# Performance work log

Hardware: AMD Instinct MI355X
Metric: run time of the kernel (lower is better)

The kernel has to match this reference:

```python
import jax, jax.numpy as jnp
import numpy as np

B, D, O = 16384, 1024, 2048
MU, LAM = 0.9, 0.1


def setup_inputs() -> dict:
    key = jax.random.key(0)
    ks = jax.random.split(key, 16)
    stdv = float(1.0 / np.sqrt(D))
    u = lambda k, shape, s: jax.random.uniform(k, shape, jnp.float32, -s, s)
    return {
        "x": jax.random.normal(ks[0], (B, D), jnp.float32),
        "x_ctx": jax.random.normal(ks[1], (B, D), jnp.float32),
        "classifier": u(ks[2], (O, D), stdv),
        "none_tensor": u(ks[3], (1, D), stdv),
        "ctx_q_w": u(ks[4], (O, D), stdv),
        "ctx_q_b": u(ks[5], (O,), stdv),
        "word_g_w": u(ks[6], (1, D), stdv),
        "word_g_b": u(ks[7], (1,), stdv),
        "tcq_w1": u(ks[8], (D, D), stdv),
        "tcq_b1": u(ks[9], (D,), stdv),
        "tcq_w2": u(ks[10], (O, D), stdv),
        "tcq_b2": u(ks[11], (O,), stdv),
        "history_input": 0.1 * jax.random.normal(ks[12], (O - 1, D), jnp.float32),
        "history_count": jax.random.randint(ks[13], (O - 1,), 0, 10),
        "labels": jax.random.randint(ks[14], (B,), 0, O),
    }


def reference(x, x_ctx, classifier, none_tensor, ctx_q_w, ctx_q_b,
              word_g_w, word_g_b, tcq_w1, tcq_b1, tcq_w2, tcq_b2,
              history_input, history_count, labels):
    mu, lam = MU, LAM
    # ---- update_history (torch.no_grad), vectorized over classes via segment_sum ----
    xs = jax.lax.stop_gradient(x)
    sums = jax.ops.segment_sum(xs, labels, num_segments=O)               # [O, D]
    counts = jax.ops.segment_sum(jnp.ones((B,), jnp.float32), labels, num_segments=O)  # [O]
    has = counts[1:] > 0                                                  # classes 1..O-1
    cls_mean = sums[1:] / jnp.maximum(counts[1:], 1.0)[:, None]
    hist = jnp.where(has[:, None], mu * history_input + cls_mean, history_input)
    cnt = history_count + has.astype(history_count.dtype)
    # ---- generate_substitute (mu < 1 branch) ----
    denom = 1.0 - jnp.power(mu, jnp.maximum(cnt, 1).astype(jnp.float32))[:, None]
    v = hist * (1.0 - mu) / denom                                        # [O-1, D]
    r_sub = jnp.concatenate([none_tensor, v], axis=0)                    # [O, D]
    ctx_logits = x_ctx @ ctx_q_w.T + ctx_q_b                              # [B, O]
    att_logits = jax.nn.gelu(x @ tcq_w1.T + tcq_b1, approximate=False) @ tcq_w2.T + tcq_b2  # [B, O]
    # ---- gated combine + bilinear classifier (training=True path: w uses ctx_logits) ----
    g_word = jax.nn.sigmoid(x @ word_g_w.T + word_g_b)                    # [B, 1]
    w = g_word * jax.nn.sigmoid(ctx_logits)                               # [B, O]
    # logits = sum(((1-w)*x[:,None,:] + w*r_sub) * classifier, -1), collapsed algebraically
    logits = (1.0 - w) * (x @ classifier.T) + w * jnp.einsum('od,od->o', r_sub, classifier)[None, :]
    # ---- losses on labels >= 0 (mask-weighted means, jit-safe) ----
    mask = (labels >= 0).astype(jnp.float32)
    n = jnp.maximum(mask.sum(), 1.0)
    lsm = jax.nn.log_softmax(logits, axis=-1)
    nll = -jnp.take_along_axis(lsm, jnp.maximum(labels, 0)[:, None], axis=1)[:, 0]
    ce = (mask * nll).sum() / n
    mse_row = jnp.mean((ctx_logits - att_logits) ** 2, axis=-1)
    mse = (mask * mse_row).sum() / n
    return (ce + lam * mse, logits)
```

## Files before the change

kernel.cpp:

```cpp
#include <hip/hip_runtime.h>
#include <cstdint>
#include <cstddef>

#define DEV __device__ __forceinline__

typedef __attribute__((ext_vector_type(4))) float f32x4;
typedef __attribute__((ext_vector_type(8))) short bf16x8;
typedef unsigned short ushort_t;
typedef __attribute__((ext_vector_type(8))) unsigned short ushort8;

static constexpr int B_ = 16384, D_ = 1024, O_ = 2048;
static constexpr float LAM_ = 0.1f;

static constexpr size_t WS_XBF   = 0;
static constexpr size_t WS_XCBF  = WS_XBF   + (size_t)B_ * D_ * 2;
static constexpr size_t WS_HBF   = WS_XCBF  + (size_t)B_ * D_ * 2;
static constexpr size_t WS_CLSBF = WS_HBF   + (size_t)B_ * D_ * 2;
static constexpr size_t WS_CTWBF = WS_CLSBF + (size_t)O_ * D_ * 2;
static constexpr size_t WS_W2BF  = WS_CTWBF + (size_t)O_ * D_ * 2;
static constexpr size_t WS_W1BF  = WS_W2BF  + (size_t)O_ * D_ * 2;
static constexpr size_t WS_SMALL = WS_W1BF  + (size_t)D_ * D_ * 2;
static constexpr size_t SM_COUNTS = 0;
static constexpr size_t SM_TSUM   = 8192;
static constexpr size_t SM_MSE    = 16384;
static constexpr size_t SM_ACCS   = 81920;
static constexpr size_t SM_ZERO_BYTES = 82176;
static constexpr size_t SM_S      = 82176;
static constexpr size_t SM_GWORD  = 90368;
static constexpr size_t SM_CEROW  = 155904;

DEV float wave_sum(float v) {
  #pragma unroll
  for (int o = 32; o; o >>= 1) v += __shfl_xor(v, o, 64);
  return v;
}

DEV ushort_t f2bf1(float f) {
  union { float f; unsigned u; } c{f};
  unsigned r = c.u + 0x7fffu + ((c.u >> 16) & 1u);
  return (ushort_t)(r >> 16);
}

DEV float sigmoidf(float z) { return 1.0f / (1.0f + expf(-z)); }

DEV void gload_lds16(const ushort_t* g, ushort_t* l) {
  __builtin_amdgcn_global_load_lds((const __attribute__((address_space(1))) void*)g,
                                   (__attribute__((address_space(3))) void*)l, 16, 0, 0);
}

DEV void stage_tile(const ushort_t* __restrict__ src, size_t ldk, ushort_t* lds, int tid) {
  int c0 = tid, c1 = tid + 256;
  gload_lds16(src + (size_t)(c0 >> 2) * ldk + (size_t)((c0 & 3) * 8), lds + c0 * 8);
  gload_lds16(src + (size_t)(c1 >> 2) * ldk + (size_t)((c1 & 3) * 8), lds + c1 * 8);
}

__global__ __launch_bounds__(256) void f2bf_kernel(const float* __restrict__ in,
                                                   ushort_t* __restrict__ out, int n8) {
  int i = blockIdx.x * 256 + threadIdx.x;
  if (i >= n8) return;
  const float4* p = (const float4*)(in + (size_t)i * 8);
  float4 a = p[0], b = p[1];
  ushort8 o;
  o[0] = f2bf1(a.x); o[1] = f2bf1(a.y); o[2] = f2bf1(a.z); o[3] = f2bf1(a.w);
  o[4] = f2bf1(b.x); o[5] = f2bf1(b.y); o[6] = f2bf1(b.z); o[7] = f2bf1(b.w);
  *(ushort8*)(out + (size_t)i * 8) = o;
}

__global__ __launch_bounds__(256) void rowdot_kernel(const float* __restrict__ x,
    const float* __restrict__ cls, const float* __restrict__ wg,
    const float* __restrict__ wgb, const int* __restrict__ labels,
    float* __restrict__ tsum, float* __restrict__ counts, float* __restrict__ g_word) {
  int wave = threadIdx.x >> 6, lane = threadIdx.x & 63;
  int row = blockIdx.x * 4 + wave;
  const float* xr = x + (size_t)row * D_;
  int lab = labels[row];
  const float* cr = cls + (size_t)max(lab, 0) * D_;
  float t = 0.f, g = 0.f;
  #pragma unroll
  for (int j = 0; j < 4; ++j) {
    int d = j * 256 + lane * 4;
    float4 xv = *(const float4*)(xr + d);
    float4 cv = *(const float4*)(cr + d);
    float4 wv = *(const float4*)(wg + d);
    t += xv.x * cv.x + xv.y * cv.y + xv.z * cv.z + xv.w * cv.w;
    g += xv.x * wv.x + xv.y * wv.y + xv.z * wv.z + xv.w * wv.w;
  }
  t = wave_sum(t); g = wave_sum(g);
  if (lane == 0) {
    if (lab >= 0) {
      atomicAdd(&tsum[lab], t);
      atomicAdd(&counts[lab], 1.0f);
    }
    g_word[row] = sigmoidf(g + wgb[0]);
  }
}

__global__ __launch_bounds__(256) void scls_kernel(const float* __restrict__ cls,
    const float* __restrict__ none_t, const float* __restrict__ hist,
    const int* __restrict__ hcnt, const float* __restrict__ counts,
    const float* __restrict__ tsum, float* __restrict__ s) {
  int wave = threadIdx.x >> 6, lane = threadIdx.x & 63;
  int o = blockIdx.x * 4 + wave;
  if (o >= O_) return;
  const float* cr = cls + (size_t)o * D_;
  const float* src = (o == 0) ? none_t : hist + (size_t)(o - 1) * D_;
  float dv = 0.f;
  #pragma unroll
  for (int j = 0; j < 4; ++j) {
    int d = j * 256 + lane * 4;
    float4 a = *(const float4*)(src + d);
    float4 c = *(const float4*)(cr + d);
    dv += a.x * c.x + a.y * c.y + a.z * c.z + a.w * c.w;
  }
  dv = wave_sum(dv);
  if (lane == 0) {
    if (o == 0) { s[0] = dv; }
    else {
      float co = counts[o];
      bool has = co > 0.f;
      int cnt = hcnt[o - 1] + (has ? 1 : 0);
      float denom = 1.f - powf(0.9f, (float)max(cnt, 1));
      float val = has ? (0.9f * dv + tsum[o] / fmaxf(co, 1.f)) : dv;
      s[o] = (0.1f / denom) * val;
    }
  }
}

__global__ __launch_bounds__(256, 3) void gemm_h_kernel(const ushort_t* __restrict__ A,
    const ushort_t* __restrict__ Bw, const float* __restrict__ bias,
    ushort_t* __restrict__ Hout) {
  __shared__ ushort_t As[128 * 32], Bs[128 * 32];
  const int tid = threadIdx.x, lane = tid & 63, wave = tid >> 6;
  const int wr = wave >> 1, wc = wave & 1;
  int bid = blockIdx.x;
  int group = bid / 64, within = bid % 64;
  int bm = group * 8 + (within % 8);
  int bn = within / 8;
  f32x4 acc[4][4] = {};
  const ushort_t* Ap = A + (size_t)bm * 128 * D_;
  const ushort_t* Bp = Bw + (size_t)bn * 128 * D_;
  for (int k0 = 0; k0 < D_; k0 += 32) {
    stage_tile(Ap + k0, D_, As, tid);
    stage_tile(Bp + k0, D_, Bs, tid);
    __syncthreads();
    bf16x8 af[4], bfr[4];
    int r = lane & 15, kq = (lane >> 4) * 8;
    #pragma unroll
    for (int m = 0; m < 4; m++) af[m] = *(const bf16x8*)&As[(wr * 64 + m * 16 + r) * 32 + kq];
    #pragma unroll
    for (int n = 0; n < 4; n++) bfr[n] = *(const bf16x8*)&Bs[(wc * 64 + n * 16 + r) * 32 + kq];
    #pragma unroll
    for (int m = 0; m < 4; m++)
      #pragma unroll
      for (int n = 0; n < 4; n++)
        acc[m][n] = __builtin_amdgcn_mfma_f32_16x16x32_bf16(af[m], bfr[n], acc[m][n], 0, 0, 0);
    __syncthreads();
  }
  #pragma unroll
  for (int m = 0; m < 4; m++)
    #pragma unroll
    for (int n = 0; n < 4; n++) {
      int col = bn * 128 + wc * 64 + n * 16 + (lane & 15);
      float bcol = bias[col];
      #pragma unroll
      for (int i = 0; i < 4; i++) {
        int row = bm * 128 + wr * 64 + m * 16 + (lane >> 4) * 4 + i;
        float v = acc[m][n][i] + bcol;
        float gl = 0.5f * v * (1.f + erff(v * 0.70710678118f));
        Hout[(size_t)row * D_ + col] = f2bf1(gl);
      }
    }
}

__global__ __launch_bounds__(256, 3) void gemm_xc_kernel(const ushort_t* __restrict__ A,
    const ushort_t* __restrict__ Bw, float* __restrict__ out1) {
  __shared__ ushort_t As[128 * 32], Bs[128 * 32];
  const int tid = threadIdx.x, lane = tid & 63, wave = tid >> 6;
  const int wr = wave >> 1, wc = wave & 1;
  int bid = blockIdx.x;
  int group = bid / 128, within = bid % 128;
  int bm = group * 8 + (within % 8);
  int bn = within / 8;
  f32x4 acc[4][4] = {};
  const ushort_t* Ap = A + (size_t)bm * 128 * D_;
  const ushort_t* Bp = Bw + (size_t)bn * 128 * D_;
  for (int k0 = 0; k0 < D_; k0 += 32) {
    stage_tile(Ap + k0, D_, As, tid);
    stage_tile(Bp + k0, D_, Bs, tid);
    __syncthreads();
    bf16x8 af[4], bfr[4];
    int r = lane & 15, kq = (lane >> 4) * 8;
    #pragma unroll
    for (int m = 0; m < 4; m++) af[m] = *(const bf16x8*)&As[(wr * 64 + m * 16 + r) * 32 + kq];
    #pragma unroll
    for (int n = 0; n < 4; n++) bfr[n] = *(const bf16x8*)&Bs[(wc * 64 + n * 16 + r) * 32 + kq];
    #pragma unroll
    for (int m = 0; m < 4; m++)
      #pragma unroll
      for (int n = 0; n < 4; n++)
        acc[m][n] = __builtin_amdgcn_mfma_f32_16x16x32_bf16(af[m], bfr[n], acc[m][n], 0, 0, 0);
    __syncthreads();
  }
  #pragma unroll
  for (int m = 0; m < 4; m++)
    #pragma unroll
    for (int n = 0; n < 4; n++) {
      int col = bn * 128 + wc * 64 + n * 16 + (lane & 15);
      #pragma unroll
      for (int i = 0; i < 4; i++) {
        int row = bm * 128 + wr * 64 + m * 16 + (lane >> 4) * 4 + i;
        out1[(size_t)row * O_ + col] = acc[m][n][i];
      }
    }
}

__global__ __launch_bounds__(256, 2) void gemm_fused_kernel(
    const ushort_t* __restrict__ Axc,
    const ushort_t* __restrict__ Bctx,
    const ushort_t* __restrict__ Ah,
    const ushort_t* __restrict__ Batt,
    const float* __restrict__ ctx_b, const float* __restrict__ b2,
    const float* __restrict__ g_word, const float* __restrict__ s,
    float* __restrict__ mse_row, float* __restrict__ out1) {
  __shared__ ushort_t As1[128 * 32], Bs1[128 * 32], As2[128 * 32], Bs2[128 * 32];
  const int tid = threadIdx.x, lane = tid & 63, wave = tid >> 6;
  const int wr = wave >> 1, wc = wave & 1;
  int bid = blockIdx.x;
  int group = bid / 128, within = bid % 128;
  int bm = group * 8 + (within % 8);
  int bn = within / 8;
  f32x4 acc1[4][4] = {}, acc2[4][4] = {};
  const ushort_t* Ap1 = Axc + (size_t)bm * 128 * D_;
  const ushort_t* Bp1 = Bctx + (size_t)bn * 128 * D_;
  const ushort_t* Ap2 = Ah + (size_t)bm * 128 * D_;
  const ushort_t* Bp2 = Batt + (size_t)bn * 128 * D_;
  for (int k0 = 0; k0 < D_; k0 += 32) {
    stage_tile(Ap1 + k0, D_, As1, tid);
    stage_tile(Bp1 + k0, D_, Bs1, tid);
    stage_tile(Ap2 + k0, D_, As2, tid);
    stage_tile(Bp2 + k0, D_, Bs2, tid);
    __syncthreads();
    int r = lane & 15, kq = (lane >> 4) * 8;
    bf16x8 a1[4], b1v[4], a2[4], b2v[4];
    #pragma unroll
    for (int m = 0; m < 4; m++) {
      a1[m] = *(const bf16x8*)&As1[(wr * 64 + m * 16 + r) * 32 + kq];
      a2[m] = *(const bf16x8*)&As2[(wr * 64 + m * 16 + r) * 32 + kq];
    }
    #pragma unroll
    for (int n = 0; n < 4; n++) {
      b1v[n] = *(const bf16x8*)&Bs1[(wc * 64 + n * 16 + r) * 32 + kq];
      b2v[n] = *(const bf16x8*)&Bs2[(wc * 64 + n * 16 + r) * 32 + kq];
    }
    #pragma unroll
    for (int m = 0; m < 4; m++)
      #pragma unroll
      for (int n = 0; n < 4; n++) {
        acc1[m][n] = __builtin_amdgcn_mfma_f32_16x16x32_bf16(a1[m], b1v[n], acc1[m][n], 0, 0, 0);
        acc2[m][n] = __builtin_amdgcn_mfma_f32_16x16x32_bf16(a2[m], b2v[n], acc2[m][n], 0, 0, 0);
      }
    __syncthreads();
  }
  #pragma unroll
  for (int m = 0; m < 4; m++) {
    #pragma unroll
    for (int i = 0; i < 4; i++) {
      int row = bm * 128 + wr * 64 + m * 16 + (lane >> 4) * 4 + i;
      float gw = g_word[row];
      float msum = 0.f;
      #pragma unroll
      for (int n = 0; n < 4; n++) {
        int col = bn * 128 + wc * 64 + n * 16 + (lane & 15);
        float ctx = acc1[m][n][i] + ctx_b[col];
        float att = acc2[m][n][i] + b2[col];
        float w = gw * sigmoidf(ctx);
        size_t off = (size_t)row * O_ + col;
        float xc = out1[off];
        out1[off] = (1.f - w) * xc + w * s[col];
        float d = ctx - att;
        msum += d * d;
      }
      #pragma unroll
      for (int o = 1; o < 16; o <<= 1) msum += __shfl_xor(msum, o, 64);
      if ((lane & 15) == 0) atomicAdd(&mse_row[row], msum);
    }
  }
}

__global__ __launch_bounds__(256) void ce_kernel(const float* __restrict__ logits,
    const int* __restrict__ labels, float* __restrict__ ce_row) {
  int row = blockIdx.x, t = threadIdx.x, lane = t & 63, wave = t >> 6;
  const float* lr = logits + (size_t)row * O_;
  float v[8];
  float m = -INFINITY;
  #pragma unroll
  for (int j = 0; j < 8; j++) { v[j] = lr[t + j * 256]; m = fmaxf(m, v[j]); }
  #pragma unroll
  for (int o = 32; o; o >>= 1) m = fmaxf(m, __shfl_xor(m, o, 64));
  __shared__ float red[8];
  if (lane == 0) red[wave] = m;
  __syncthreads();
  m = fmaxf(fmaxf(red[0], red[1]), fmaxf(red[2], red[3]));
  float se = 0.f;
  #pragma unroll
  for (int j = 0; j < 8; j++) se += expf(v[j] - m);
  se = wave_sum(se);
  if (lane == 0) red[4 + wave] = se;
  __syncthreads();
  if (t == 0) {
    float bs = red[4] + red[5] + red[6] + red[7];
    int lab = labels[row];
    float nll = 0.f;
    if (lab >= 0) nll = -(lr[lab] - m - logf(bs));
    ce_row[row] = nll;
  }
}

__global__ __launch_bounds__(256) void finalize_kernel(const float* __restrict__ ce_row,
    const float* __restrict__ mse_row, const int* __restrict__ labels,
    float* __restrict__ out0) {
  int t = threadIdx.x, lane = t & 63, wave = t >> 6;
  float sn = 0.f, sm = 0.f, sc = 0.f;
  for (int i = t; i < B_; i += 256) {
    if (labels[i] >= 0) { sn += ce_row[i]; sm += mse_row[i]; sc += 1.f; }
  }
  sn = wave_sum(sn); sm = wave_sum(sm); sc = wave_sum(sc);
  __shared__ float r0[4], r1[4], r2[4];
  if (lane == 0) { r0[wave] = sn; r1[wave] = sm; r2[wave] = sc; }
  __syncthreads();
  if (t == 0) {
    float a = r0[0] + r0[1] + r0[2] + r0[3];
    float b = r1[0] + r1[1] + r1[2] + r1[3];
    float c = r2[0] + r2[1] + r2[2] + r2[3];
    out0[0] = (a + LAM_ * (b / (float)O_)) / fmaxf(c, 1.f);
  }
}

extern "C" void kernel_launch(void* const* d_in, const int* in_sizes, int n_in,
                              void* d_out, int out_size, void* d_ws, size_t ws_size,
                              hipStream_t stream) {
  const float* x        = (const float*)d_in[0];
  const float* x_ctx    = (const float*)d_in[1];
  const float* cls      = (const float*)d_in[2];
  const float* none_t   = (const float*)d_in[3];
  const float* ctx_q_w  = (const float*)d_in[4];
  const float* ctx_q_b  = (const float*)d_in[5];
  const float* word_g_w = (const float*)d_in[6];
  const float* word_g_b = (const float*)d_in[7];
  const float* w1       = (const float*)d_in[8];
  const float* b1       = (const float*)d_in[9];
  const float* w2       = (const float*)d_in[10];
  const float* b2       = (const float*)d_in[11];
  const float* hist     = (const float*)d_in[12];
  const int*   hcnt     = (const int*)d_in[13];
  const int*   labels   = (const int*)d_in[14];

  float* out  = (float*)d_out;
  float* out1 = out + 1;
  char* ws = (char*)d_ws;

  ushort_t* xbf   = (ushort_t*)(ws + WS_XBF);
  ushort_t* xcbf  = (ushort_t*)(ws + WS_XCBF);
  ushort_t* hbf   = (ushort_t*)(ws + WS_HBF);
  ushort_t* clsbf = (ushort_t*)(ws + WS_CLSBF);
  ushort_t* ctwbf = (ushort_t*)(ws + WS_CTWBF);
  ushort_t* w2bf  = (ushort_t*)(ws + WS_W2BF);
  ushort_t* w1bf  = (ushort_t*)(ws + WS_W1BF);
  float* counts   = (float*)(ws + WS_SMALL + SM_COUNTS);
  float* tsum     = (float*)(ws + WS_SMALL + SM_TSUM);
  float* mse_row  = (float*)(ws + WS_SMALL + SM_MSE);
  float* s        = (float*)(ws + WS_SMALL + SM_S);
  float* g_word   = (float*)(ws + WS_SMALL + SM_GWORD);
  float* ce_row   = (float*)(ws + WS_SMALL + SM_CEROW);

  hipMemsetAsync(ws + WS_SMALL, 0, SM_ZERO_BYTES, stream);

  f2bf_kernel<<<8192, 256, 0, stream>>>(x, xbf, B_ * D_ / 8);
  f2bf_kernel<<<8192, 256, 0, stream>>>(x_ctx, xcbf, B_ * D_ / 8);
  f2bf_kernel<<<1024, 256, 0, stream>>>(cls, clsbf, O_ * D_ / 8);
  f2bf_kernel<<<1024, 256, 0, stream>>>(ctx_q_w, ctwbf, O_ * D_ / 8);
  f2bf_kernel<<<1024, 256, 0, stream>>>(w2, w2bf, O_ * D_ / 8);
  f2bf_kernel<<<512, 256, 0, stream>>>(w1, w1bf, D_ * D_ / 8);

  rowdot_kernel<<<B_ / 4, 256, 0, stream>>>(x, cls, word_g_w, word_g_b, labels,
                                            tsum, counts, g_word);
  scls_kernel<<<O_ / 4, 256, 0, stream>>>(cls, none_t, hist, hcnt, counts, tsum, s);

  gemm_h_kernel<<<(B_ / 128) * (D_ / 128), 256, 0, stream>>>(xbf, w1bf, b1, hbf);
  gemm_xc_kernel<<<(B_ / 128) * (O_ / 128), 256, 0, stream>>>(xbf, clsbf, out1);
  gemm_fused_kernel<<<(B_ / 128) * (O_ / 128), 256, 0, stream>>>(
      xcbf, ctwbf, hbf, w2bf, ctx_q_b, b2, g_word, s, mse_row, out1);

  ce_kernel<<<B_, 256, 0, stream>>>(out1, labels, ce_row);
  finalize_kernel<<<1, 256, 0, stream>>>(ce_row, mse_row, labels, out);
}
```

Measured before the change: 507.2 us.

## Replace GEMMs with 256x256 multi-stage pipelined template kernel and split fused GEMM

Replaces the three 128x128 single-buffered GEMM kernels with one templated 256x256-tile, 512-thread kernel. It uses a 4-slot LDS ring filled by direct global-to-LDS loads, explicit vmcnt waits, barriers and MFMA priority hints to overlap loads with compute. The former fused ctx/att GEMM is split into separate passes whose epilogues go through out1: ctx logits are stored first, att reads them for MSE, and the classifier pass applies the gate. This gives larger tiles and deeper pipelining in exchange for extra global traffic on the logits buffer and more kernel launches.

New measurement: 472.8 us. 6.8% less time.

```diff
diff --git a/kernel.cpp b/kernel.cpp
--- a/kernel.cpp
+++ b/kernel.cpp
@@ -23,7 +23,6 @@
 static constexpr size_t SM_COUNTS = 0;
 static constexpr size_t SM_TSUM   = 8192;
 static constexpr size_t SM_MSE    = 16384;
-static constexpr size_t SM_ACCS   = 81920;
 static constexpr size_t SM_ZERO_BYTES = 82176;
 static constexpr size_t SM_S      = 82176;
 static constexpr size_t SM_GWORD  = 90368;
@@ -48,10 +47,13 @@
                                    (__attribute__((address_space(3))) void*)l, 16, 0, 0);
 }
 
-DEV void stage_tile(const ushort_t* __restrict__ src, size_t ldk, ushort_t* lds, int tid) {
-  int c0 = tid, c1 = tid + 256;
-  gload_lds16(src + (size_t)(c0 >> 2) * ldk + (size_t)((c0 & 3) * 8), lds + c0 * 8);
-  gload_lds16(src + (size_t)(c1 >> 2) * ldk + (size_t)((c1 & 3) * 8), lds + c1 * 8);
+DEV void stage2(const ushort_t* __restrict__ s0, ushort_t* slot, int tid) {
+  gload_lds16(s0, slot + tid * 8);
+  gload_lds16(s0 + 128 * 1024, slot + (tid + 512) * 8);
+}
+
+DEV f32x4 mfma16(bf16x8 a, bf16x8 b, f32x4 c) {
+  return __builtin_amdgcn_mfma_f32_16x16x32_bf16(a, b, c, 0, 0, 0);
 }
 
 __global__ __launch_bounds__(256) void f2bf_kernel(const float* __restrict__ in,
@@ -126,163 +128,136 @@
   }
 }
 
-__global__ __launch_bounds__(256, 3) void gemm_h_kernel(const ushort_t* __restrict__ A,
-    const ushort_t* __restrict__ Bw, const float* __restrict__ bias,
-    ushort_t* __restrict__ Hout) {
-  __shared__ ushort_t As[128 * 32], Bs[128 * 32];
+template<bool S01, bool S23, int W1, int W3>
+DEV void tile8(int t, const ushort_t* __restrict__ sA0, const ushort_t* __restrict__ sB0,
+               ushort_t* lds, int tid, int aoff, int boff, f32x4 (&acc)[8][4]) {
+  const int k0 = 2 * t, k1 = 2 * t + 1;
+  const ushort_t* As0 = lds + (k0 & 3) * 8192;
+  const ushort_t* Bs0 = lds + 32768 + (k0 & 3) * 8192;
+  const ushort_t* As1 = lds + (k1 & 3) * 8192;
+  const ushort_t* Bs1 = lds + 32768 + (k1 & 3) * 8192;
+  bf16x8 afr[4], bfr[4];
+  #pragma unroll
+  for (int n = 0; n < 4; n++) bfr[n] = *(const bf16x8*)&Bs0[boff + n * 512];
+  #pragma unroll
+  for (int m = 0; m < 4; m++) afr[m] = *(const bf16x8*)&As0[aoff + m * 512];
+  if constexpr (S01) stage2(sA0 + (size_t)(2 * t + 3) * 32, lds + ((2 * t + 3) & 3) * 8192, tid);
+  __builtin_amdgcn_s_barrier();
+  __builtin_amdgcn_s_setprio(1);
+  #pragma unroll
+  for (int m = 0; m < 4; m++)
+    #pragma unroll
+    for (int n = 0; n < 4; n++) acc[m][n] = mfma16(afr[m], bfr[n], acc[m][n]);
+  __builtin_amdgcn_s_setprio(0);
+  __builtin_amdgcn_s_barrier();
+  #pragma unroll
+  for (int m = 0; m < 4; m++) afr[m] = *(const bf16x8*)&As0[aoff + (m + 4) * 512];
+  if constexpr (S01) stage2(sB0 + (size_t)(2 * t + 3) * 32, lds + 32768 + ((2 * t + 3) & 3) * 8192, tid);
+  __builtin_amdgcn_s_barrier();
+  __builtin_amdgcn_s_setprio(1);
+  #pragma unroll
+  for (int m = 0; m < 4; m++)
+    #pragma unroll
+    for (int n = 0; n < 4; n++) acc[m + 4][n] = mfma16(afr[m], bfr[n], acc[m + 4][n]);
+  __builtin_amdgcn_s_setprio(0);
+  if constexpr (W1 == 4) asm volatile("s_waitcnt vmcnt(4)" ::: "memory");
+  else if constexpr (W1 == 2) asm volatile("s_waitcnt vmcnt(2)" ::: "memory");
+  else if constexpr (W1 == 0) asm volatile("s_waitcnt vmcnt(0)" ::: "memory");
+  __builtin_amdgcn_s_barrier();
+  #pragma unroll
+  for (int n = 0; n < 4; n++) bfr[n] = *(const bf16x8*)&Bs1[boff + n * 512];
+  #pragma unroll
+  for (int m = 0; m < 4; m++) afr[m] = *(const bf16x8*)&As1[aoff + m * 512];
+  if constexpr (S23) stage2(sA0 + (size_t)(2 * t + 4) * 32, lds + ((2 * t + 4) & 3) * 8192, tid);
+  __builtin_amdgcn_s_barrier();
+  __builtin_amdgcn_s_setprio(1);
+  #pragma unroll
+  for (int m = 0; m < 4; m++)
+    #pragma unroll
+    for (int n = 0; n < 4; n++) acc[m][n] = mfma16(afr[m], bfr[n], acc[m][n]);
+  __builtin_amdgcn_s_setprio(0);
+  __builtin_amdgcn_s_barrier();
+  #pragma unroll
+  for (int m = 0; m < 4; m++) afr[m] = *(const bf16x8*)&As1[aoff + (m + 4) * 512];
+  if constexpr (S23) stage2(sB0 + (size_t)(2 * t + 4) * 32, lds + 32768 + ((2 * t + 4) & 3) * 8192, tid);
+  __builtin_amdgcn_s_barrier();
+  __builtin_amdgcn_s_setprio(1);
+  #pragma unroll
+  for (int m = 0; m < 4; m++)
+    #pragma unroll
+    for (int n = 0; n < 4; n++) acc[m + 4][n] = mfma16(afr[m], bfr[n], acc[m + 4][n]);
+  __builtin_amdgcn_s_setprio(0);
+  if constexpr (W3 == 4) asm volatile("s_waitcnt vmcnt(4)" ::: "memory");
+  else if constexpr (W3 == 2) asm volatile("s_waitcnt vmcnt(2)" ::: "memory");
+  else if constexpr (W3 == 0) asm volatile("s_waitcnt vmcnt(0)" ::: "memory");
+  __builtin_amdgcn_s_barrier();
+}
+
+template<int EPI, int NTSHIFT>
+__global__ __launch_bounds__(512, 2) void gemm8_kernel(
+    const ushort_t* __restrict__ A, const ushort_t* __restrict__ Bmat,
+    const float* __restrict__ bias, float* __restrict__ fout,
+    ushort_t* __restrict__ hout, const float* __restrict__ g_word,
+    const float* __restrict__ svec, float* __restrict__ mse_row) {
+  __shared__ __align__(16) ushort_t lds[65536];
   const int tid = threadIdx.x, lane = tid & 63, wave = tid >> 6;
-  const int wr = wave >> 1, wc = wave & 1;
+  const int wr = wave >> 2, wc = wave & 3;
+  const int nwg = 64 << NTSHIFT, cpx = nwg >> 3;
   int bid = blockIdx.x;
-  int group = bid / 64, within = bid % 64;
-  int bm = group * 8 + (within % 8);
-  int bn = within / 8;
-  f32x4 acc[4][4] = {};
-  const ushort_t* Ap = A + (size_t)bm * 128 * D_;
-  const ushort_t* Bp = Bw + (size_t)bn * 128 * D_;
-  for (int k0 = 0; k0 < D_; k0 += 32) {
-    stage_tile(Ap + k0, D_, As, tid);
-    stage_tile(Bp + k0, D_, Bs, tid);
-    __syncthreads();
-    bf16x8 af[4], bfr[4];
-    int r = lane & 15, kq = (lane >> 4) * 8;
-    #pragma unroll
-    for (int m = 0; m < 4; m++) af[m] = *(const bf16x8*)&As[(wr * 64 + m * 16 + r) * 32 + kq];
-    #pragma unroll
-    for (int n = 0; n < 4; n++) bfr[n] = *(const bf16x8*)&Bs[(wc * 64 + n * 16 + r) * 32 + kq];
-    #pragma unroll
-    for (int m = 0; m < 4; m++)
-      #pragma unroll
-      for (int n = 0; n < 4; n++)
-        acc[m][n] = __builtin_amdgcn_mfma_f32_16x16x32_bf16(af[m], bfr[n], acc[m][n], 0, 0, 0);
-    __syncthreads();
-  }
-  #pragma unroll
-  for (int m = 0; m < 4; m++)
-    #pragma unroll
-    for (int n = 0; n < 4; n++) {
-      int col = bn * 128 + wc * 64 + n * 16 + (lane & 15);
-      float bcol = bias[col];
-      #pragma unroll
-      for (int i = 0; i < 4; i++) {
-        int row = bm * 128 + wr * 64 + m * 16 + (lane >> 4) * 4 + i;
-        float v = acc[m][n][i] + bcol;
-        float gl = 0.5f * v * (1.f + erff(v * 0.70710678118f));
-        Hout[(size_t)row * D_ + col] = f2bf1(gl);
-      }
-    }
-}
-
-__global__ __launch_bounds__(256, 3) void gemm_xc_kernel(const ushort_t* __restrict__ A,
-    const ushort_t* __restrict__ Bw, float* __restrict__ out1) {
-  __shared__ ushort_t As[128 * 32], Bs[128 * 32];
-  const int tid = threadIdx.x, lane = tid & 63, wave = tid >> 6;
-  const int wr = wave >> 1, wc = wave & 1;
-  int bid = blockIdx.x;
-  int group = bid / 128, within = bid % 128;
-  int bm = group * 8 + (within % 8);
-  int bn = within / 8;
-  f32x4 acc[4][4] = {};
-  const ushort_t* Ap = A + (size_t)bm * 128 * D_;
-  const ushort_t* Bp = Bw + (size_t)bn * 128 * D_;
-  for (int k0 = 0; k0 < D_; k0 += 32) {
-    stage_tile(Ap + k0, D_, As, tid);
-    stage_tile(Bp + k0, D_, Bs, tid);
-    __syncthreads();
-    bf16x8 af[4], bfr[4];
-    int r = lane & 15, kq = (lane >> 4) * 8;
-    #pragma unroll
-    for (int m = 0; m < 4; m++) af[m] = *(const bf16x8*)&As[(wr * 64 + m * 16 + r) * 32 + kq];
-    #pragma unroll
-    for (int n = 0; n < 4; n++) bfr[n] = *(const bf16x8*)&Bs[(wc * 64 + n * 16 + r) * 32 + kq];
-    #pragma unroll
-    for (int m = 0; m < 4; m++)
-      #pragma unroll
-      for (int n = 0; n < 4; n++)
-        acc[m][n] = __builtin_amdgcn_mfma_f32_16x16x32_bf16(af[m], bfr[n], acc[m][n], 0, 0, 0);
-    __syncthreads();
-  }
-  #pragma unroll
-  for (int m = 0; m < 4; m++)
-    #pragma unroll
-    for (int n = 0; n < 4; n++) {
-      int col = bn * 128 + wc * 64 + n * 16 + (lane & 15);
-      #pragma unroll
-      for (int i = 0; i < 4; i++) {
-        int row = bm * 128 + wr * 64 + m * 16 + (lane >> 4) * 4 + i;
-        out1[(size_t)row * O_ + col] = acc[m][n][i];
-      }
-    }
-}
-
-__global__ __launch_bounds__(256, 2) void gemm_fused_kernel(
-    const ushort_t* __restrict__ Axc,
-    const ushort_t* __restrict__ Bctx,
-    const ushort_t* __restrict__ Ah,
-    const ushort_t* __restrict__ Batt,
-    const float* __restrict__ ctx_b, const float* __restrict__ b2,
-    const float* __restrict__ g_word, const float* __restrict__ s,
-    float* __restrict__ mse_row, float* __restrict__ out1) {
-  __shared__ ushort_t As1[128 * 32], Bs1[128 * 32], As2[128 * 32], Bs2[128 * 32];
-  const int tid = threadIdx.x, lane = tid & 63, wave = tid >> 6;
-  const int wr = wave >> 1, wc = wave & 1;
-  int bid = blockIdx.x;
-  int group = bid / 128, within = bid % 128;
-  int bm = group * 8 + (within % 8);
-  int bn = within / 8;
-  f32x4 acc1[4][4] = {}, acc2[4][4] = {};
-  const ushort_t* Ap1 = Axc + (size_t)bm * 128 * D_;
-  const ushort_t* Bp1 = Bctx + (size_t)bn * 128 * D_;
-  const ushort_t* Ap2 = Ah + (size_t)bm * 128 * D_;
-  const ushort_t* Bp2 = Batt + (size_t)bn * 128 * D_;
-  for (int k0 = 0; k0 < D_; k0 += 32) {
-    stage_tile(Ap1 + k0, D_, As1, tid);
-    stage_tile(Bp1 + k0, D_, Bs1, tid);
-    stage_tile(Ap2 + k0, D_, As2, tid);
-    stage_tile(Bp2 + k0, D_, Bs2, tid);
-    __syncthreads();
-    int r = lane & 15, kq = (lane >> 4) * 8;
-    bf16x8 a1[4], b1v[4], a2[4], b2v[4];
-    #pragma unroll
-    for (int m = 0; m < 4; m++) {
-      a1[m] = *(const bf16x8*)&As1[(wr * 64 + m * 16 + r) * 32 + kq];
-      a2[m] = *(const bf16x8*)&As2[(wr * 64 + m * 16 + r) * 32 + kq];
-    }
-    #pragma unroll
-    for (int n = 0; n < 4; n++) {
-      b1v[n] = *(const bf16x8*)&Bs1[(wc * 64 + n * 16 + r) * 32 + kq];
-      b2v[n] = *(const bf16x8*)&Bs2[(wc * 64 + n * 16 + r) * 32 + kq];
-    }
-    #pragma unroll
-    for (int m = 0; m < 4; m++)
+  int wg = (bid & 7) * cpx + (bid >> 3);
+  const int bm = wg >> NTSHIFT, bn = wg & ((1 << NTSHIFT) - 1);
+  const int NCOL = 256 << NTSHIFT;
+  const ushort_t* sA0 = A + ((size_t)bm * 256 + (tid >> 2)) * 1024 + (tid & 3) * 8;
+  const ushort_t* sB0 = Bmat + ((size_t)bn * 256 + (tid >> 2)) * 1024 + (tid & 3) * 8;
+  const int aoff = (wr * 128 + (lane & 15)) * 32 + (lane >> 4) * 8;
+  const int boff = (wc * 64 + (lane & 15)) * 32 + (lane >> 4) * 8;
+  f32x4 acc[8][4] = {};
+  stage2(sA0, lds, tid);
+  stage2(sB0, lds + 32768, tid);
+  stage2(sA0 + 32, lds + 8192, tid);
+  stage2(sB0 + 32, lds + 32768 + 8192, tid);
+  stage2(sA0 + 64, lds + 2 * 8192, tid);
+  stage2(sB0 + 64, lds + 32768 + 2 * 8192, tid);
+  asm volatile("s_waitcnt vmcnt(4)" ::: "memory");
+  __builtin_amdgcn_s_barrier();
+  for (int t = 0; t < 14; ++t)
+    tile8<true, true, 4, 4>(t, sA0, sB0, lds, tid, aoff, boff, acc);
+  tile8<true, false, 4, 2>(14, sA0, sB0, lds, tid, aoff, boff, acc);
+  tile8<false, false, 0, -1>(15, sA0, sB0, lds, tid, aoff, boff, acc);
+  #pragma unroll
+  for (int m = 0; m < 8; m++) {
+    #pragma unroll
+    for (int i = 0; i < 4; i++) {
+      int row = bm * 256 + wr * 128 + m * 16 + (lane >> 4) * 4 + i;
+      float gw = 0.f, msum = 0.f;
+      if constexpr (EPI == 3) gw = g_word[row];
       #pragma unroll
       for (int n = 0; n < 4; n++) {
-        acc1[m][n] = __builtin_amdgcn_mfma_f32_16x16x32_bf16(a1[m], b1v[n], acc1[m][n], 0, 0, 0);
-        acc2[m][n] = __builtin_amdgcn_mfma_f32_16x16x32_bf16(a2[m], b2v[n], acc2[m][n], 0, 0, 0);
+        int col = bn * 256 + wc * 64 + n * 16 + (lane & 15);
+        float v = acc[m][n][i];
+        if constexpr (EPI == 0) {
+          float z = v + bias[col];
+          float gl = 0.5f * z * (1.f + erff(z * 0.70710678118f));
+          hout[(size_t)row * 1024 + col] = f2bf1(gl);
+        } else if constexpr (EPI == 1) {
+          fout[(size_t)row * NCOL + col] = v + bias[col];
+        } else if constexpr (EPI == 2) {
+          float att = v + bias[col];
+          float ctx = fout[(size_t)row * NCOL + col];
+          float d = ctx - att;
+          msum += d * d;
+        } else {
+          size_t off = (size_t)row * NCOL + col;
+          float ctx = fout[off];
+          float w = gw * sigmoidf(ctx);
+          fout[off] = (1.f - w) * v + w * svec[col];
+        }
       }
-    __syncthreads();
-  }
-  #pragma unroll
-  for (int m = 0; m < 4; m++) {
-    #pragma unroll
-    for (int i = 0; i < 4; i++) {
-      int row = bm * 128 + wr * 64 + m * 16 + (lane >> 4) * 4 + i;
-      float gw = g_word[row];
-      float msum = 0.f;
-      #pragma unroll
-      for (int n = 0; n < 4; n++) {
-        int col = bn * 128 + wc * 64 + n * 16 + (lane & 15);
-        float ctx = acc1[m][n][i] + ctx_b[col];
-        float att = acc2[m][n][i] + b2[col];
-        float w = gw * sigmoidf(ctx);
-        size_t off = (size_t)row * O_ + col;
-        float xc = out1[off];
-        out1[off] = (1.f - w) * xc + w * s[col];
-        float d = ctx - att;
-        msum += d * d;
+      if constexpr (EPI == 2) {
+        #pragma unroll
+        for (int o = 1; o < 16; o <<= 1) msum += __shfl_xor(msum, o, 64);
+        if ((lane & 15) == 0) atomicAdd(&mse_row[row], msum);
       }
-      #pragma unroll
-      for (int o = 1; o < 16; o <<= 1) msum += __shfl_xor(msum, o, 64);
-      if ((lane & 15) == 0) atomicAdd(&mse_row[row], msum);
     }
   }
 }
@@ -386,10 +361,14 @@
                                             tsum, counts, g_word);
   scls_kernel<<<O_ / 4, 256, 0, stream>>>(cls, none_t, hist, hcnt, counts, tsum, s);
 
-  gemm_h_kernel<<<(B_ / 128) * (D_ / 128), 256, 0, stream>>>(xbf, w1bf, b1, hbf);
-  gemm_xc_kernel<<<(B_ / 128) * (O_ / 128), 256, 0, stream>>>(xbf, clsbf, out1);
-  gemm_fused_kernel<<<(B_ / 128) * (O_ / 128), 256, 0, stream>>>(
-      xcbf, ctwbf, hbf, w2bf, ctx_q_b, b2, g_word, s, mse_row, out1);
+  gemm8_kernel<0, 2><<<64 * 4, 512, 0, stream>>>(xbf, w1bf, b1, nullptr, hbf,
+                                                 nullptr, nullptr, nullptr);
+  gemm8_kernel<1, 3><<<64 * 8, 512, 0, stream>>>(xcbf, ctwbf, ctx_q_b, out1, nullptr,
+                                                 nullptr, nullptr, nullptr);
+  gemm8_kernel<2, 3><<<64 * 8, 512, 0, stream>>>(hbf, w2bf, b2, out1, nullptr,
+                                                 nullptr, nullptr, mse_row);
+  gemm8_kernel<3, 3><<<64 * 8, 512, 0, stream>>>(xbf, clsbf, nullptr, out1, nullptr,
+                                                 g_word, s, nullptr);
 
   ce_kernel<<<B_, 256, 0, stream>>>(out1, labels, ce_row);
   finalize_kernel<<<1, 256, 0, stream>>>(ce_row, mse_row, labels, out);
```
